# Performance work log

Measured on AMD Instinct MI355X. Metric: run time of the kernel, lower is better.

Reference implementation:

```python
import jax, jax.numpy as jnp
import numpy as np

N_ENT = 100000
N_USR = 50000
N_REL = 16
D = 64
E_KG = 1500000
E_CF = 1500000
N_LAYERS = 3
LEAKY_SLOPE = 0.01  # torch nn.LeakyReLU default


def setup_inputs() -> dict:
    key = jax.random.key(0)
    ks = jax.random.split(key, 14)
    inv = 1.0 / np.sqrt(D)
    return {
        "ent_user_embed": jax.random.normal(ks[0], (N_ENT + N_USR, D), jnp.float32) * inv,
        "rel_embed": jax.random.normal(ks[1], (N_REL, D), jnp.float32) * inv,
        "Wk_w": jax.random.normal(ks[2], (2 * D, D), jnp.float32) * (1.0 / np.sqrt(2 * D)),
        "Wk_b": jnp.zeros((D,), jnp.float32),
        "Wa_w": jax.random.normal(ks[3], (D, D), jnp.float32) * inv,
        "Wb_w": jax.random.normal(ks[4], (D, D), jnp.float32) * inv,
        "kg_h": jax.random.randint(ks[5], (E_KG,), 0, N_ENT, jnp.int32),
        "kg_t": jax.random.randint(ks[6], (E_KG,), 0, N_ENT, jnp.int32),
        "kg_r": jax.random.randint(ks[7], (E_KG,), 0, N_REL, jnp.int32),
        "ain_row": jax.random.randint(ks[8], (E_CF,), 0, N_ENT + N_USR, jnp.int32),
        "ain_col": jax.random.randint(ks[9], (E_CF,), 0, N_ENT + N_USR, jnp.int32),
        "ain_val": jax.random.uniform(ks[10], (E_CF,), jnp.float32) * (1.0 / 64.0),
        "user_ids": jax.random.randint(ks[11], (1024,), 0, N_USR, jnp.int32) + N_ENT,
        "item_ids": jax.random.randint(ks[12], (2048,), 0, N_ENT, jnp.int32),
        "n_entities": N_ENT,
        "n_users": N_USR,
    }


def reference(ent_user_embed, rel_embed, Wk_w, Wk_b, Wa_w, Wb_w,
              kg_h, kg_t, kg_r, ain_row, ain_col, ain_val,
              user_ids, item_ids, n_entities, n_users):
    # ---- update_attention: per-edge KG attention + sparse row-softmax ----
    h_e = ent_user_embed[kg_h]          # [E, D] gather
    t_e = ent_user_embed[kg_t]          # [E, D] gather
    r_e = rel_embed[kg_r]               # [E, D]
    trans = jnp.concatenate([t_e, h_e], axis=1) @ Wk_w + Wk_b  # W_k([t||h])
    logits = jnp.sum(trans * r_e, axis=1)                      # [E]
    logits = jnp.where(logits >= 0, logits, LEAKY_SLOPE * logits)
    row_max = jax.ops.segment_max(logits, kg_h, num_segments=n_entities)
    ex = jnp.exp(logits - row_max[kg_h])
    row_sum = jax.ops.segment_sum(ex, kg_h, num_segments=n_entities)
    attn = ex / row_sum[kg_h]           # sparse softmax over dim=1 (per head row)

    n_total = n_entities + n_users

    def spmm_kg(x):   # A_kg @ x, A_kg is [n_ent, n_ent] COO with attn values
        return jax.ops.segment_sum(attn[:, None] * x[kg_t], kg_h, num_segments=n_entities)

    def spmm_ain(x):  # A_in @ x, [n_total, n_total] COO
        return jax.ops.segment_sum(ain_val[:, None] * x[ain_col], ain_row, num_segments=n_total)

    def fusion_gate(kg_embed, ig_embed):
        g = jax.nn.sigmoid(kg_embed @ Wa_w + ig_embed @ Wb_w)
        return g * kg_embed + (1.0 - g) * ig_embed

    # ---- get_embeddings: L layers of dual propagation + gated fusion ----
    e_entities = ent_user_embed[:n_entities]
    e_users = ent_user_embed[n_entities:]
    user_sum = e_users
    item_sum = e_entities
    e_items_dual = e_entities
    e_users_curr = e_users
    e_entities_curr = e_entities
    for _ in range(N_LAYERS):
        e_items_kg = spmm_kg(e_entities_curr)
        ig_input = jnp.concatenate([e_items_dual, e_users_curr], axis=0)
        ig_output = spmm_ain(ig_input)
        e_items_collab = ig_output[:n_entities]
        e_users_new = ig_output[n_entities:]
        e_items_dual = fusion_gate(e_items_kg, e_items_collab)
        item_sum = item_sum + e_items_collab
        user_sum = user_sum + e_users_new
        e_users_curr = e_users_new
        e_entities_curr = e_items_kg
        # mess_dropout = [0,0,0] (eval mode): no-op
    all_embed = jnp.concatenate([item_sum, user_sum], axis=0)  # [n_total, D]

    # ---- calc_score ----
    return all_embed[user_ids] @ all_embed[item_ids].T  # [n_u, n_i]
```

## Files before the change

kernel.cpp:

```cpp
#include <hip/hip_runtime.h>
#include <math.h>

#define N_ENT 100000
#define N_USR 50000
#define N_TOT 150000
#define N_ROWS 250000
#define DD 64

#define SCAN_BLK 256
#define SCAN_ITEMS 1024

#define SORT_T 4096
#define BUK_SHIFT 8
#define NBUKU 977
#define LDSCAP 5120

typedef _Float16 half8 __attribute__((ext_vector_type(8)));
typedef _Float16 half4 __attribute__((ext_vector_type(4)));
typedef _Float16 h2v __attribute__((ext_vector_type(2)));
typedef float floatx4 __attribute__((ext_vector_type(4)));

__global__ void k_rel(const float* __restrict__ Wk_w, const float* __restrict__ Wk_b,
                      const float* __restrict__ rel, float* __restrict__ uvr) {
    int r = blockIdx.x;
    int k = threadIdx.x;
    const float* rv = rel + r * DD;
    const float* wrow = Wk_w + k * DD;
    float s = 0.f;
    for (int j = 0; j < DD; ++j) s += wrow[j] * rv[j];
    uvr[r * 132 + k] = s;
    if (k == 0) {
        float c = 0.f;
        for (int j = 0; j < DD; ++j) c += Wk_b[j] * rv[j];
        uvr[r * 132 + 128] = c;
    }
}

__global__ void k_uvpack(const float* __restrict__ uvr, _Float16* __restrict__ upack) {
    int i = blockIdx.x * 256 + threadIdx.x;
    if (i >= 2048) return;
    int kstep = i >> 10;
    int rem = i & 1023;
    int ntile = rem >> 9;
    int rem2 = rem & 511;
    int lane = rem2 >> 3;
    int j = rem2 & 7;
    int k = kstep * 32 + (lane >> 4) * 8 + j;
    upack[i] = (_Float16)uvr[(lane & 15) * 132 + ntile * 64 + k];
}

__global__ __launch_bounds__(256) void k_proj(const _Float16* __restrict__ e16,
        const _Float16* __restrict__ upack, float* __restrict__ Puv) {
    int lane = threadIdx.x & 63;
    int wv = (blockIdx.x * 256 + threadIdx.x) >> 6;
    int row0 = wv * 16;
    if (row0 >= N_ENT) return;
    int m = lane & 15;
    int quad = lane >> 4;

    const _Float16* er = e16 + (size_t)(row0 + m) * DD + quad * 8;
    half8 a0 = *(const half8*)(er);
    half8 a1 = *(const half8*)(er + 32);

    const half8* up = (const half8*)upack;
    half8 b00 = up[0 * 128 + 0 * 64 + lane];
    half8 b01 = up[0 * 128 + 1 * 64 + lane];
    half8 b10 = up[1 * 128 + 0 * 64 + lane];
    half8 b11 = up[1 * 128 + 1 * 64 + lane];

    floatx4 c0 = {0.f, 0.f, 0.f, 0.f};
    floatx4 c1 = {0.f, 0.f, 0.f, 0.f};
    c0 = __builtin_amdgcn_mfma_f32_16x16x32_f16(a0, b00, c0, 0, 0, 0);
    c0 = __builtin_amdgcn_mfma_f32_16x16x32_f16(a1, b10, c0, 0, 0, 0);
    c1 = __builtin_amdgcn_mfma_f32_16x16x32_f16(a0, b01, c1, 0, 0, 0);
    c1 = __builtin_amdgcn_mfma_f32_16x16x32_f16(a1, b11, c1, 0, 0, 0);

#pragma unroll
    for (int r = 0; r < 4; ++r) {
        size_t row = (size_t)(row0 + quad * 4 + r);
        Puv[row * 32 + m] = c0[r];
        Puv[row * 32 + 16 + m] = c1[r];
    }
}

__global__ __launch_bounds__(256) void k_sort_hist(const int* __restrict__ kg_h,
        const int* __restrict__ ain_row, int* __restrict__ tilecnt,
        int E_KG, int E_TOT, int NT) {
    __shared__ int hist[1024];
#pragma unroll
    for (int k = 0; k < 4; ++k) hist[k * 256 + threadIdx.x] = 0;
    __syncthreads();
    int tile = blockIdx.x;
    int base = tile * SORT_T;
#pragma unroll
    for (int k = 0; k < SORT_T / 256; ++k) {
        int e = base + k * 256 + threadIdx.x;
        if (e < E_TOT) {
            int row = (e < E_KG) ? kg_h[e] : (N_ENT + ain_row[e - E_KG]);
            atomicAdd(&hist[row >> BUK_SHIFT], 1);
        }
    }
    __syncthreads();
    for (int b = threadIdx.x; b < NBUKU; b += 256)
        tilecnt[b * NT + tile] = hist[b];
}

__global__ __launch_bounds__(SCAN_BLK) void k_blocksum(const int* __restrict__ cnt,
                                                       int* __restrict__ bsum, int n) {
    __shared__ int s[SCAN_BLK];
    int base = blockIdx.x * SCAN_ITEMS;
    int sum = 0;
    for (int i = threadIdx.x; i < SCAN_ITEMS; i += SCAN_BLK) {
        int idx = base + i;
        if (idx < n) sum += cnt[idx];
    }
    s[threadIdx.x] = sum;
    __syncthreads();
    for (int off = SCAN_BLK / 2; off; off >>= 1) {
        if (threadIdx.x < off) s[threadIdx.x] += s[threadIdx.x + off];
        __syncthreads();
    }
    if (threadIdx.x == 0) bsum[blockIdx.x] = s[0];
}

__global__ __launch_bounds__(1024) void k_bscan(int* __restrict__ bsum, int nb,
                                                int* __restrict__ total_out) {
    __shared__ int s[1024];
    int tid = threadIdx.x;
    int v = (tid < nb) ? bsum[tid] : 0;
    s[tid] = v;
    __syncthreads();
    for (int off = 1; off < 1024; off <<= 1) {
        int t = (tid >= off) ? s[tid - off] : 0;
        __syncthreads();
        s[tid] += t;
        __syncthreads();
    }
    if (tid < nb) bsum[tid] = s[tid] - v;
    if (tid == 1023) *total_out = s[1023];
}

__global__ __launch_bounds__(SCAN_BLK) void k_scan_apply(const int* __restrict__ cnt,
        int* __restrict__ scanned, const int* __restrict__ bsum, int n) {
    __shared__ int s[SCAN_BLK];
    int base = blockIdx.x * SCAN_ITEMS;
    int t = threadIdx.x;
    int idx0 = base + t * 4;
    int v[4];
    int lsum = 0;
#pragma unroll
    for (int k = 0; k < 4; ++k) {
        int idx = idx0 + k;
        v[k] = (idx < n) ? cnt[idx] : 0;
        lsum += v[k];
    }
    s[t] = lsum;
    __syncthreads();
    for (int off = 1; off < SCAN_BLK; off <<= 1) {
        int tv = (t >= off) ? s[t - off] : 0;
        __syncthreads();
        s[t] += tv;
        __syncthreads();
    }
    int pre = (t ? s[t - 1] : 0) + bsum[blockIdx.x];
#pragma unroll
    for (int k = 0; k < 4; ++k) {
        int idx = idx0 + k;
        if (idx < n) scanned[idx] = pre;
        pre += v[k];
    }
}

__global__ __launch_bounds__(256) void k_sort_scatter(const int* __restrict__ kg_h,
        const int* __restrict__ kg_t, const int* __restrict__ kg_r,
        const int* __restrict__ ain_row, const int* __restrict__ ain_col,
        const float* __restrict__ ain_val, const int* __restrict__ tilescan,
        int2* __restrict__ bufA, int E_KG, int E_TOT, int NT) {
    __shared__ int2 seg[SORT_T];
    __shared__ short sbuk[SORT_T];
    __shared__ int hist[1024];
    __shared__ int cur[1024];
    __shared__ int ssum[256];
    int tid = threadIdx.x;
    int tile = blockIdx.x;
#pragma unroll
    for (int k = 0; k < 4; ++k) hist[k * 256 + tid] = 0;
    __syncthreads();

    int base = tile * SORT_T;
    int px[SORT_T / 256], py[SORT_T / 256];
    short pb[SORT_T / 256];
#pragma unroll
    for (int k = 0; k < SORT_T / 256; ++k) {
        int e = base + k * 256 + tid;
        int x = 0, y = 0, b = -1;
        if (e < E_TOT) {
            int row;
            if (e < E_KG) {
                row = kg_h[e];
                x = kg_t[e] | (kg_r[e] << 17) | ((row & 255) << 22);
                y = 0;
            } else {
                int i = e - E_KG;
                row = N_ENT + ain_row[i];
                x = ain_col[i] | ((row & 255) << 22);
                y = __float_as_int(ain_val[i]);
            }
            b = row >> BUK_SHIFT;
            atomicAdd(&hist[b], 1);
        }
        px[k] = x; py[k] = y; pb[k] = (short)b;
    }
    __syncthreads();

    {
        int b0 = 4 * tid;
        int v0 = hist[b0], v1 = hist[b0 + 1], v2 = hist[b0 + 2], v3 = hist[b0 + 3];
        int g0 = (b0     < NBUKU) ? tilescan[(b0    ) * NT + tile] : 0;
        int g1 = (b0 + 1 < NBUKU) ? tilescan[(b0 + 1) * NT + tile] : 0;
        int g2 = (b0 + 2 < NBUKU) ? tilescan[(b0 + 2) * NT + tile] : 0;
        int g3 = (b0 + 3 < NBUKU) ? tilescan[(b0 + 3) * NT + tile] : 0;
        int lsum = v0 + v1 + v2 + v3;
        ssum[tid] = lsum;
        __syncthreads();
        for (int off = 1; off < 256; off <<= 1) {
            int t = (tid >= off) ? ssum[tid - off] : 0;
            __syncthreads();
            ssum[tid] += t;
            __syncthreads();
        }
        int ex = ssum[tid] - lsum;
        cur[b0] = ex;     hist[b0] = g0 - ex;     ex += v0;
        cur[b0 + 1] = ex; hist[b0 + 1] = g1 - ex; ex += v1;
        cur[b0 + 2] = ex; hist[b0 + 2] = g2 - ex; ex += v2;
        cur[b0 + 3] = ex; hist[b0 + 3] = g3 - ex;
    }
    __syncthreads();

#pragma unroll
    for (int k = 0; k < SORT_T / 256; ++k) {
        if (pb[k] >= 0) {
            int slot = atomicAdd(&cur[pb[k]], 1);
            seg[slot] = make_int2(px[k], py[k]);
            sbuk[slot] = pb[k];
        }
    }
    __syncthreads();

    int cnt = min(SORT_T, E_TOT - base);
    for (int i = tid; i < cnt; i += 256) {
        int b = sbuk[i];
        bufA[hist[b] + i] = seg[i];
    }
}

__global__ __launch_bounds__(256) void k_sort_fine(const int* __restrict__ tilescan,
        const int2* __restrict__ bufA, int2* __restrict__ pairbuf,
        int* __restrict__ rowptr, const float* __restrict__ Puv,
        const float* __restrict__ uvr, int NT) {
    __shared__ int2 seg[LDSCAP];
    __shared__ int rcnt[256];
    __shared__ int rexc[256];
    __shared__ int rcur[256];
    __shared__ float rsum[256];
    __shared__ float c16[16];
    int tid = threadIdx.x;
    int b = blockIdx.x;
    rcnt[tid] = 0;
    rsum[tid] = 0.f;
    if (tid < 16) c16[tid] = uvr[tid * 132 + 128];
    __syncthreads();

    int base = tilescan[b * NT];
    int endo = tilescan[(b + 1) * NT];
    int bsize = endo - base;
    int growbase = b << BUK_SHIFT;

    for (int i = base + tid; i < endo; i += 256) {
        unsigned rlow = ((unsigned)bufA[i].x) >> 22;
        atomicAdd(&rcnt[rlow], 1);
    }
    __syncthreads();

    {
        int v = rcnt[tid];
        rexc[tid] = v;
        __syncthreads();
        for (int off = 1; off < 256; off <<= 1) {
            int t = (tid >= off) ? rexc[tid - off] : 0;
            __syncthreads();
            rexc[tid] += t;
            __syncthreads();
        }
        int ex = rexc[tid] - v;
        rexc[tid] = ex;
        rcur[tid] = ex;
        int row = growbase + tid;
        if (row <= N_ROWS) rowptr[row] = base + ex;
    }
    __syncthreads();

    if (bsize <= LDSCAP) {
        for (int i = base + tid; i < endo; i += 256) {
            int2 p = bufA[i];
            unsigned rlow = ((unsigned)p.x) >> 22;
            seg[atomicAdd(&rcur[rlow], 1)] = p;
        }
        __syncthreads();
        for (int i = tid; i < bsize; i += 256) {
            int2 p = seg[i];
            unsigned rlow = ((unsigned)p.x) >> 22;
            int grow = growbase + (int)rlow;
            if (grow < N_ENT) {
                int t = p.x & 0x1FFFF;
                int r = (p.x >> 17) & 15;
                float lg = Puv[(size_t)t * 32 + r] + Puv[(size_t)grow * 32 + 16 + r] + c16[r];
                lg = lg >= 0.f ? lg : 0.01f * lg;
                float exv = expf(lg);
                seg[i].y = __float_as_int(exv);
                atomicAdd(&rsum[rlow], exv);
            }
        }
        __syncthreads();
        rsum[tid] = 1.f / rsum[tid];
        __syncthreads();
        for (int i = tid; i < bsize; i += 256) {
            int2 p = seg[i];
            unsigned rlow = ((unsigned)p.x) >> 22;
            if (growbase + (int)rlow < N_ENT)
                p.y = __float_as_int(__int_as_float(p.y) * rsum[rlow]);
            pairbuf[base + i] = p;
        }
    } else {
        for (int i = base + tid; i < endo; i += 256) {
            int2 p = bufA[i];
            unsigned rlow = ((unsigned)p.x) >> 22;
            int slot = atomicAdd(&rcur[rlow], 1);
            pairbuf[base + slot] = p;
        }
        __syncthreads();
        for (int i = base + tid; i < endo; i += 256) {
            int2 p = pairbuf[i];
            unsigned rlow = ((unsigned)p.x) >> 22;
            int grow = growbase + (int)rlow;
            if (grow < N_ENT) {
                int t = p.x & 0x1FFFF;
                int r = (p.x >> 17) & 15;
                float lg = Puv[(size_t)t * 32 + r] + Puv[(size_t)grow * 32 + 16 + r] + c16[r];
                lg = lg >= 0.f ? lg : 0.01f * lg;
                float exv = expf(lg);
                pairbuf[i].y = __float_as_int(exv);
                atomicAdd(&rsum[rlow], exv);
            }
        }
        __syncthreads();
        rsum[tid] = 1.f / rsum[tid];
        __syncthreads();
        for (int i = base + tid; i < endo; i += 256) {
            int2 p = pairbuf[i];
            unsigned rlow = ((unsigned)p.x) >> 22;
            if (growbase + (int)rlow < N_ENT)
                pairbuf[i].y = __float_as_int(__int_as_float(p.y) * rsum[rlow]);
        }
    }
}

__global__ void k_wcvt(const float* __restrict__ Wa, const float* __restrict__ Wb,
                       _Float16* __restrict__ wpack) {
    int i = blockIdx.x * 256 + threadIdx.x;
    if (i >= 8192) return;
    int m = i >> 12;
    int rem = i & 4095;
    int kstep = rem >> 11;
    int rem2 = rem & 2047;
    int ntile = rem2 >> 9;
    int rem3 = rem2 & 511;
    int lane = rem3 >> 3;
    int j = rem3 & 7;
    int k = kstep * 32 + (lane >> 4) * 8 + j;
    int n = ntile * 16 + (lane & 15);
    const float* W = m ? Wb : Wa;
    wpack[i] = (_Float16)W[k * 64 + n];
}

__global__ __launch_bounds__(256) void k_spmm_u(const int* __restrict__ rowptr,
        const int2* __restrict__ pairbuf, const _Float16* __restrict__ x,
        _Float16* __restrict__ outbuf, int row_begin, int row_end, int cmask) {
    int wid0 = (blockIdx.x * 256 + threadIdx.x) >> 6;
    int wpair = __builtin_amdgcn_readfirstlane(wid0);
    int lane = threadIdx.x & 63;
    int half = lane >> 5;
    int sub = lane & 31;
    int row = row_begin + wpair * 2 + half;
    if (row >= row_end) return;
    int d0 = sub * 2;
    const _Float16* xb = x + d0;
    int s = rowptr[row], e = rowptr[row + 1];
    float a00 = 0.f, a01 = 0.f, a10 = 0.f, a11 = 0.f;
    float a20 = 0.f, a21 = 0.f, a30 = 0.f, a31 = 0.f;
    int i = s;
    for (; i + 4 <= e; i += 4) {
        int2 p0 = pairbuf[i], p1 = pairbuf[i + 1], p2 = pairbuf[i + 2], p3 = pairbuf[i + 3];
        h2v g0 = *(const h2v*)(xb + (size_t)(p0.x & cmask) * DD);
        h2v g1 = *(const h2v*)(xb + (size_t)(p1.x & cmask) * DD);
        h2v g2 = *(const h2v*)(xb + (size_t)(p2.x & cmask) * DD);
        h2v g3 = *(const h2v*)(xb + (size_t)(p3.x & cmask) * DD);
        float w0 = __int_as_float(p0.y), w1 = __int_as_float(p1.y);
        float w2 = __int_as_float(p2.y), w3 = __int_as_float(p3.y);
        a00 = fmaf(w0, (float)g0[0], a00); a01 = fmaf(w0, (float)g0[1], a01);
        a10 = fmaf(w1, (float)g1[0], a10); a11 = fmaf(w1, (float)g1[1], a11);
        a20 = fmaf(w2, (float)g2[0], a20); a21 = fmaf(w2, (float)g2[1], a21);
        a30 = fmaf(w3, (float)g3[0], a30); a31 = fmaf(w3, (float)g3[1], a31);
    }
    for (; i < e; ++i) {
        int2 p = pairbuf[i];
        h2v g = *(const h2v*)(xb + (size_t)(p.x & cmask) * DD);
        float w = __int_as_float(p.y);
        a00 = fmaf(w, (float)g[0], a00); a01 = fmaf(w, (float)g[1], a01);
    }
    float r0 = (a00 + a10) + (a20 + a30);
    float r1 = (a01 + a11) + (a21 + a31);
    h2v st; st[0] = (_Float16)r0; st[1] = (_Float16)r1;
    *(h2v*)(outbuf + (size_t)(row - row_begin) * DD + d0) = st;
}

__global__ __launch_bounds__(256) void k_gate3(const _Float16* __restrict__ kg16,
        const _Float16* __restrict__ ig16, const _Float16* __restrict__ wpack,
        _Float16* __restrict__ dual16, int ngate) {
    __shared__ _Float16 sw[8192];
    if ((int)blockIdx.x >= ngate) {
        int i = ((int)blockIdx.x - ngate) * 256 + threadIdx.x;
        if (i < N_USR * DD / 8) {
            size_t o = (size_t)N_ENT * DD / 8 + i;
            ((half8*)dual16)[o] = ((const half8*)ig16)[o];
        }
        return;
    }
    for (int i = threadIdx.x * 8; i < 8192; i += 256 * 8)
        *(half8*)(sw + i) = *(const half8*)(wpack + i);
    __syncthreads();
    int lane = threadIdx.x & 63;
    int wv = (blockIdx.x * 256 + threadIdx.x) >> 6;
    int row0 = wv * 16;
    if (row0 >= N_ENT) return;
    int m = lane & 15;
    int quad = lane >> 4;

    const _Float16* kgr = kg16 + (size_t)(row0 + m) * DD + quad * 8;
    const _Float16* igr = ig16 + (size_t)(row0 + m) * DD + quad * 8;
    half8 akg0 = *(const half8*)(kgr);
    half8 akg1 = *(const half8*)(kgr + 32);
    half8 aig0 = *(const half8*)(igr);
    half8 aig1 = *(const half8*)(igr + 32);

    floatx4 acc[4];
#pragma unroll
    for (int t = 0; t < 4; ++t) {
        half8 bA0 = *(const half8*)(sw + 0 * 4096 + 0 * 2048 + t * 512 + lane * 8);
        half8 bA1 = *(const half8*)(sw + 0 * 4096 + 1 * 2048 + t * 512 + lane * 8);
        half8 bB0 = *(const half8*)(sw + 1 * 4096 + 0 * 2048 + t * 512 + lane * 8);
        half8 bB1 = *(const half8*)(sw + 1 * 4096 + 1 * 2048 + t * 512 + lane * 8);
        floatx4 c = {0.f, 0.f, 0.f, 0.f};
        c = __builtin_amdgcn_mfma_f32_16x16x32_f16(akg0, bA0, c, 0, 0, 0);
        c = __builtin_amdgcn_mfma_f32_16x16x32_f16(akg1, bA1, c, 0, 0, 0);
        c = __builtin_amdgcn_mfma_f32_16x16x32_f16(aig0, bB0, c, 0, 0, 0);
        c = __builtin_amdgcn_mfma_f32_16x16x32_f16(aig1, bB1, c, 0, 0, 0);
        acc[t] = c;
    }

#pragma unroll
    for (int t = 0; t < 4; ++t) {
#pragma unroll
        for (int r = 0; r < 4; ++r) {
            int row = quad * 4 + r;
            int col = t * 16 + m;
            size_t o = (size_t)(row0 + row) * DD + col;
            float kv = (float)kg16[o];
            float cv = (float)ig16[o];
            float g = 1.f / (1.f + expf(-acc[t][r]));
            dual16[o] = (_Float16)(g * kv + (1.f - g) * cv);
        }
    }
}

__global__ void k_init(const float* __restrict__ embed, _Float16* __restrict__ dual16) {
    int i = blockIdx.x * blockDim.x + threadIdx.x;
    if (i >= N_TOT * DD) return;
    dual16[i] = (_Float16)embed[i];
}

__global__ __launch_bounds__(256) void k_out(const float* __restrict__ embed,
        const _Float16* __restrict__ ig0, const _Float16* __restrict__ ig1,
        const _Float16* __restrict__ ig2, const int* __restrict__ user_ids,
        const int* __restrict__ item_ids, float* __restrict__ out) {
    __shared__ float uvec[32 * DD];
    int ug = blockIdx.x >> 3;
    int qi = blockIdx.x & 7;
    int ub = ug * 32;
    for (int i = threadIdx.x; i < 32 * DD; i += 256) {
        int uu = i >> 6, d = i & 63;
        size_t o = (size_t)user_ids[ub + uu] * DD + d;
        uvec[i] = embed[o] + (float)ig0[o] + (float)ig1[o] + (float)ig2[o];
    }
    __syncthreads();
    int jbase = qi * 256;
    for (int j = threadIdx.x; j < 256; j += 256) {
        size_t ro = (size_t)item_ids[jbase + j] * DD;
        float acc[32];
#pragma unroll
        for (int u = 0; u < 32; ++u) acc[u] = 0.f;
        for (int d = 0; d < DD; d += 4) {
            float4 ev = *(const float4*)(embed + ro + d);
            half4 h0 = *(const half4*)(ig0 + ro + d);
            half4 h1 = *(const half4*)(ig1 + ro + d);
            half4 h2 = *(const half4*)(ig2 + ro + d);
            float iv0 = ev.x + (float)h0[0] + (float)h1[0] + (float)h2[0];
            float iv1 = ev.y + (float)h0[1] + (float)h1[1] + (float)h2[1];
            float iv2 = ev.z + (float)h0[2] + (float)h1[2] + (float)h2[2];
            float iv3 = ev.w + (float)h0[3] + (float)h1[3] + (float)h2[3];
#pragma unroll
            for (int u = 0; u < 32; ++u) {
                acc[u] = fmaf(iv0, uvec[u * DD + d + 0], acc[u]);
                acc[u] = fmaf(iv1, uvec[u * DD + d + 1], acc[u]);
                acc[u] = fmaf(iv2, uvec[u * DD + d + 2], acc[u]);
                acc[u] = fmaf(iv3, uvec[u * DD + d + 3], acc[u]);
            }
        }
#pragma unroll
        for (int u = 0; u < 32; ++u)
            out[(size_t)(ub + u) * 2048 + jbase + j] = acc[u];
    }
}

extern "C" void kernel_launch(void* const* d_in, const int* in_sizes, int n_in,
                              void* d_out, int out_size, void* d_ws, size_t ws_size,
                              hipStream_t stream) {
    const float* embed   = (const float*)d_in[0];
    const float* rel     = (const float*)d_in[1];
    const float* Wk_w    = (const float*)d_in[2];
    const float* Wk_b    = (const float*)d_in[3];
    const float* Wa      = (const float*)d_in[4];
    const float* Wb      = (const float*)d_in[5];
    const int*   kg_h    = (const int*)d_in[6];
    const int*   kg_t    = (const int*)d_in[7];
    const int*   kg_r    = (const int*)d_in[8];
    const int*   ain_row = (const int*)d_in[9];
    const int*   ain_col = (const int*)d_in[10];
    const float* ain_val = (const float*)d_in[11];
    const int*   user_ids = (const int*)d_in[12];
    const int*   item_ids = (const int*)d_in[13];
    int E_KG = in_sizes[6];
    int E_CF = in_sizes[9];
    int E_TOT = E_KG + E_CF;
    float* out = (float*)d_out;

    int NT  = (E_TOT + SORT_T - 1) / SORT_T;
    int NTC = NBUKU * NT;

    float* ws = (float*)d_ws;
    size_t off = 0;
    float* uvr       = ws + off; off += 16 * 132;
    float* Puv       = ws + off; off += (size_t)N_ENT * 32;
    int*   rowptr    = (int*)(ws + off); off += N_ROWS + 4;
    int*   tilecnt   = (int*)(ws + off); off += (size_t)NTC + 4;
    int*   tilescan  = (int*)(ws + off); off += (size_t)NTC + 4;
    int*   bsum      = (int*)(ws + off); off += 1024;
    int2*  pairbuf   = (int2*)(ws + off); off += 2 * (size_t)E_TOT;
    _Float16* dual16 = (_Float16*)(ws + off); off += (size_t)N_TOT * DD / 2;
    _Float16* ig16_0 = (_Float16*)(ws + off); off += (size_t)N_TOT * DD / 2;
    _Float16* ig16_1 = (_Float16*)(ws + off); off += (size_t)N_TOT * DD / 2;
    _Float16* ig16_2 = (_Float16*)(ws + off); off += (size_t)N_TOT * DD / 2;
    _Float16* kg16A  = (_Float16*)(ws + off); off += (size_t)N_ENT * DD / 2;
    _Float16* kg16B  = (_Float16*)(ws + off); off += (size_t)N_ENT * DD / 2;
    _Float16* wpack  = (_Float16*)(ws + off); off += 8192 / 2;
    int2*  bufA      = (int2*)kg16A;
    _Float16* upack  = (_Float16*)pairbuf;
    _Float16* ig_l[3] = {ig16_0, ig16_1, ig16_2};

    hipLaunchKernelGGL(k_init, dim3((N_TOT * DD + 255) / 256), dim3(256), 0, stream,
                       embed, dual16);
    hipLaunchKernelGGL(k_rel, dim3(16), dim3(128), 0, stream, Wk_w, Wk_b, rel, uvr);
    hipLaunchKernelGGL(k_uvpack, dim3(8), dim3(256), 0, stream, uvr, upack);
    hipLaunchKernelGGL(k_proj, dim3((N_ENT / 16 + 3) / 4), dim3(256), 0, stream,
                       dual16, upack, Puv);

    hipLaunchKernelGGL(k_sort_hist, dim3(NT), dim3(256), 0, stream,
                       kg_h, ain_row, tilecnt, E_KG, E_TOT, NT);
    int nb = (NTC + SCAN_ITEMS - 1) / SCAN_ITEMS;
    hipLaunchKernelGGL(k_blocksum, dim3(nb), dim3(SCAN_BLK), 0, stream, tilecnt, bsum, NTC);
    hipLaunchKernelGGL(k_bscan, dim3(1), dim3(1024), 0, stream, bsum, nb, tilescan + NTC);
    hipLaunchKernelGGL(k_scan_apply, dim3(nb), dim3(SCAN_BLK), 0, stream,
                       tilecnt, tilescan, bsum, NTC);
    hipLaunchKernelGGL(k_sort_scatter, dim3(NT), dim3(256), 0, stream,
                       kg_h, kg_t, kg_r, ain_row, ain_col, ain_val, tilescan,
                       bufA, E_KG, E_TOT, NT);
    hipLaunchKernelGGL(k_sort_fine, dim3(NBUKU), dim3(256), 0, stream,
                       tilescan, bufA, pairbuf, rowptr, Puv, uvr, NT);

    hipLaunchKernelGGL(k_wcvt, dim3(32), dim3(256), 0, stream, Wa, Wb, wpack);

    const _Float16* cur16 = dual16;
    _Float16* kg16o = kg16A;
    _Float16* kg16alt = kg16B;
    int kg_blocks = ((N_ENT / 2) * 64 + 255) / 256;
    int cf_blocks = ((N_TOT / 2) * 64 + 255) / 256;
    int ngate = (N_ENT / 16 + 3) / 4;
    int nuc = (N_USR * DD / 8 + 255) / 256;
    for (int layer = 0; layer < 3; ++layer) {
        if (layer < 2) {
            hipLaunchKernelGGL(k_spmm_u, dim3(kg_blocks), dim3(256), 0, stream,
                               rowptr, pairbuf, cur16, kg16o, 0, N_ENT, 0x1FFFF);
            hipLaunchKernelGGL(k_spmm_u, dim3(cf_blocks), dim3(256), 0, stream,
                               rowptr, pairbuf, dual16, ig_l[layer], N_ENT, N_ROWS, 0x3FFFF);
            hipLaunchKernelGGL(k_gate3, dim3(ngate + nuc), dim3(256), 0, stream,
                               kg16o, ig_l[layer], wpack, dual16, ngate);
            cur16 = kg16o;
            kg16o = kg16alt;
            kg16alt = (_Float16*)cur16;
        } else {
            hipLaunchKernelGGL(k_spmm_u, dim3(cf_blocks), dim3(256), 0, stream,
                               rowptr, pairbuf, dual16, ig_l[layer], N_ENT, N_ROWS, 0x3FFFF);
        }
    }

    hipLaunchKernelGGL(k_out, dim3(256), dim3(256), 0, stream,
                       embed, ig16_0, ig16_1, ig16_2, user_ids, item_ids, out);
}
```

Baseline: 562.3 us.

## Sub-sort CSR edges within each row by column tile for gather locality

The fine sort stage now buckets each row's edges by a coarse column tile (column index >> 14, 8 tiles) as well as by row. Within a row, edges come out grouped by column range, so the later SpMM gathers touch nearby embedding rows closer together in time. In exchange the per-block histogram grows eightfold in LDS and each edge pays extra mask and tile arithmetic during sorting.

```diff
diff --git a/kernel.cpp b/kernel.cpp
--- a/kernel.cpp
+++ b/kernel.cpp
@@ -14,6 +14,9 @@
 #define BUK_SHIFT 8
 #define NBUKU 977
 #define LDSCAP 5120
+
+#define NTILE 8
+#define NKEY (256 * NTILE)
 
 typedef _Float16 half8 __attribute__((ext_vector_type(8)));
 typedef _Float16 half4 __attribute__((ext_vector_type(4)));
@@ -259,14 +262,15 @@
         int* __restrict__ rowptr, const float* __restrict__ Puv,
         const float* __restrict__ uvr, int NT) {
     __shared__ int2 seg[LDSCAP];
-    __shared__ int rcnt[256];
-    __shared__ int rexc[256];
-    __shared__ int rcur[256];
+    __shared__ int kcnt[NKEY];
+    __shared__ int kcur[NKEY];
+    __shared__ int ssum[256];
     __shared__ float rsum[256];
     __shared__ float c16[16];
     int tid = threadIdx.x;
     int b = blockIdx.x;
-    rcnt[tid] = 0;
+#pragma unroll
+    for (int k = 0; k < NTILE; ++k) kcnt[k * 256 + tid] = 0;
     rsum[tid] = 0.f;
     if (tid < 16) c16[tid] = uvr[tid * 132 + 128];
     __syncthreads();
@@ -277,26 +281,32 @@
     int growbase = b << BUK_SHIFT;
 
     for (int i = base + tid; i < endo; i += 256) {
-        unsigned rlow = ((unsigned)bufA[i].x) >> 22;
-        atomicAdd(&rcnt[rlow], 1);
+        int x = bufA[i].x;
+        unsigned rlow = ((unsigned)x) >> 22;
+        int mask = (growbase + (int)rlow < N_ENT) ? 0x1FFFF : 0x3FFFF;
+        int ctile = min((x & mask) >> 14, NTILE - 1);
+        atomicAdd(&kcnt[(int)rlow * NTILE + ctile], 1);
     }
     __syncthreads();
 
     {
-        int v = rcnt[tid];
-        rexc[tid] = v;
+        int v[NTILE];
+        int lsum = 0;
+#pragma unroll
+        for (int j = 0; j < NTILE; ++j) { v[j] = kcnt[tid * NTILE + j]; lsum += v[j]; }
+        ssum[tid] = lsum;
         __syncthreads();
         for (int off = 1; off < 256; off <<= 1) {
-            int t = (tid >= off) ? rexc[tid - off] : 0;
+            int t = (tid >= off) ? ssum[tid - off] : 0;
             __syncthreads();
-            rexc[tid] += t;
+            ssum[tid] += t;
             __syncthreads();
         }
-        int ex = rexc[tid] - v;
-        rexc[tid] = ex;
-        rcur[tid] = ex;
+        int ex = ssum[tid] - lsum;
         int row = growbase + tid;
         if (row <= N_ROWS) rowptr[row] = base + ex;
+#pragma unroll
+        for (int j = 0; j < NTILE; ++j) { kcur[tid * NTILE + j] = ex; ex += v[j]; }
     }
     __syncthreads();
 
@@ -304,7 +314,9 @@
         for (int i = base + tid; i < endo; i += 256) {
             int2 p = bufA[i];
             unsigned rlow = ((unsigned)p.x) >> 22;
-            seg[atomicAdd(&rcur[rlow], 1)] = p;
+            int mask = (growbase + (int)rlow < N_ENT) ? 0x1FFFF : 0x3FFFF;
+            int ctile = min((p.x & mask) >> 14, NTILE - 1);
+            seg[atomicAdd(&kcur[(int)rlow * NTILE + ctile], 1)] = p;
         }
         __syncthreads();
         for (int i = tid; i < bsize; i += 256) {
@@ -335,7 +347,9 @@
         for (int i = base + tid; i < endo; i += 256) {
             int2 p = bufA[i];
             unsigned rlow = ((unsigned)p.x) >> 22;
-            int slot = atomicAdd(&rcur[rlow], 1);
+            int mask = (growbase + (int)rlow < N_ENT) ? 0x1FFFF : 0x3FFFF;
+            int ctile = min((p.x & mask) >> 14, NTILE - 1);
+            int slot = atomicAdd(&kcur[(int)rlow * NTILE + ctile], 1);
             pairbuf[base + slot] = p;
         }
         __syncthreads();
```

Result: no change. 568.4 us (+1.1%).
